# Kernel optimization log

Measured on AMD Instinct MI355X. Metric: run time of the kernel, lower is better.

The kernel has to match this reference:

```python
import jax, jax.numpy as jnp
import numpy as np

B, L, D = 64, 256, 768
LABELS = 200
REL_OFF = 256  # to_pos[k] = k + 256


def setup_inputs() -> dict:
    key = jax.random.key(0)
    ks = jax.random.split(key, 8)
    return {
        "sequence_output": jax.random.normal(ks[0], (B, L, D), dtype=jnp.float32),
        "pos_embedding": jax.random.normal(ks[1], (2 * REL_OFF + 1, D), dtype=jnp.float32) * 0.02,
        "class_embedding": jax.random.normal(ks[2], (LABELS + 1, D), dtype=jnp.float32) * 0.02,
        "W": jax.random.normal(ks[3], (LABELS, 3 * D), dtype=jnp.float32) * 0.02,
        "b": jnp.zeros((LABELS,), dtype=jnp.float32),
        "head_indexes": jax.random.randint(ks[4], (B, L), 0, L),
        "frame": jax.random.randint(ks[5], (B,), 0, LABELS + 1),
        "pos": jax.random.randint(ks[6], (B,), 0, L),
    }


def reference(sequence_output, pos_embedding, class_embedding, W, b, head_indexes, frame, pos):
    # per-batch gather of token rows: sequence_output[i] = sequence_output[i][head_indexes[i]]
    gathered = jnp.take_along_axis(sequence_output, head_indexes[:, :, None], axis=1)  # [B,L,D]

    j = jnp.arange(sequence_output.shape[1])  # [L]
    rel = j[None, :] - pos[:, None] + REL_OFF  # [B,L] in [0, 512]
    pe = pos_embedding[rel]  # [B,L,D]

    # frame embedding only at j == pos[i], else class_embedding[0]
    fe_hit = class_embedding[frame]  # [B,D]
    is_pos = (j[None, :] == pos[:, None])[:, :, None]  # [B,L,1]
    fe = jnp.where(is_pos, fe_hit[:, None, :], class_embedding[0][None, None, :])  # [B,L,D]

    feat = jnp.concatenate([gathered, pe, fe], axis=-1)  # [B,L,3D]
    # dropout is identity at inference; classifier linear
    return jnp.einsum("blf,cf->blc", feat, W) + b
```

## Files before the change

### kernel.cpp

```cpp
#include <hip/hip_runtime.h>
#include <stdint.h>


typedef __attribute__((ext_vector_type(8))) short short8;
typedef __attribute__((ext_vector_type(4))) float f32x4;

#define AS1 __attribute__((address_space(1)))
#define AS3 __attribute__((address_space(3)))

#define NSEQ_G 1572864
#define NPE_G  49248
#define NCE_G  19296
#define NW16_G 73728
#define SEQB_OFF 0
#define PEB_OFF  12582912
#define CEB_OFF  (PEB_OFF + 393984)
#define WP_OFF   (CEB_OFF + 154368)
#define WS_ELEMS (WP_OFF + 589824)
#define WS_NEED  ((size_t)WS_ELEMS * 2)
#define TILE_STRIDE 36864

__device__ __forceinline__ unsigned short f2bf(float f) {
    union { float f; unsigned int u; } v; v.f = f;
    unsigned int u = v.u;
    return (unsigned short)((u + 0x7fffu + ((u >> 16) & 1u)) >> 16);
}

__device__ __forceinline__ short8 pack8(f32x4 a, f32x4 b) {
    short8 r;
    r[0] = (short)f2bf(a.x); r[1] = (short)f2bf(a.y);
    r[2] = (short)f2bf(a.z); r[3] = (short)f2bf(a.w);
    r[4] = (short)f2bf(b.x); r[5] = (short)f2bf(b.y);
    r[6] = (short)f2bf(b.z); r[7] = (short)f2bf(b.w);
    return r;
}

__device__ __forceinline__ void dma16(const unsigned short* g, AS3 unsigned short* l) {
    __builtin_amdgcn_global_load_lds((AS1 const unsigned int*)g,
                                     (AS3 unsigned int*)l, 16, 0, 0);
}

__global__ void prep_kernel(const float* __restrict__ seq,
                            const float* __restrict__ pe,
                            const float* __restrict__ ce,
                            const float* __restrict__ W,
                            unsigned short* __restrict__ ws) {
    int g = blockIdx.x * 256 + threadIdx.x;
    if (g < NSEQ_G) {
        const float* p = seq + (size_t)g * 8;
        *(short8*)(ws + SEQB_OFF + (size_t)g * 8) =
            pack8(*(const f32x4*)p, *(const f32x4*)(p + 4));
        return;
    }
    g -= NSEQ_G;
    if (g < NPE_G) {
        const float* p = pe + (size_t)g * 8;
        *(short8*)(ws + PEB_OFF + (size_t)g * 8) =
            pack8(*(const f32x4*)p, *(const f32x4*)(p + 4));
        return;
    }
    g -= NPE_G;
    if (g < NCE_G) {
        const float* p = ce + (size_t)g * 8;
        *(short8*)(ws + CEB_OFF + (size_t)g * 8) =
            pack8(*(const f32x4*)p, *(const f32x4*)(p + 4));
        return;
    }
    g -= NCE_G;
    if (g < NW16_G) {
        int n   = g & 15;
        int kb8 = (g >> 4) % 288;
        int t   = g / (288 * 16);
        int row = t * 16 + n;
        int col = kb8 * 8;
        f32x4 a = {0.f, 0.f, 0.f, 0.f}, b = {0.f, 0.f, 0.f, 0.f};
        if (row < 200) {
            const float* p = W + (size_t)row * 2304 + col;
            a = *(const f32x4*)p;
            b = *(const f32x4*)(p + 4);
        }
        *(short8*)(ws + WP_OFF + (size_t)g * 8) = pack8(a, b);
    }
}

__global__ __launch_bounds__(512) void gemm6_kernel(
    const unsigned short* __restrict__ ws,
    const float* __restrict__ bias,
    const int*   __restrict__ head,
    const int*   __restrict__ frame,
    const int*   __restrict__ pos,
    float* __restrict__ out)
{
    __shared__ unsigned short lds[8192 + 16384];

    const unsigned short* seqb = ws + SEQB_OFF;
    const unsigned short* peb  = ws + PEB_OFF;
    const unsigned short* ceb  = ws + CEB_OFF;
    const unsigned short* Wp   = ws + WP_OFF;

    const int tid  = threadIdx.x;
    const int wave = tid >> 6;
    const int lane = tid & 63;
    const int n16  = lane & 15;
    const int quad = lane >> 4;

    const int mblk = blockIdx.x & 255;
    const int h    = blockIdx.x >> 8;

    const int i       = mblk >> 2;
    const int pos_i   = pos[i];
    const int frame_i = frame[i];

    const int smf = wave & 3;
    const int skb = (wave >> 2) * 2;
    const int srow = mblk * 64 + smf * 16 + n16;
    const unsigned short* aSt[3];
    {
        const int sj   = srow & 255;
        const int shi  = head[srow];
        const int srel = sj - pos_i + 256;
        const int scls = (sj == pos_i) ? frame_i : 0;
        const int loff = quad * 8;
        aSt[0] = seqb + ((size_t)i * 256 + (size_t)shi) * 768 + loff;
        aSt[1] = peb + (size_t)srel * 768 + loff;
        aSt[2] = ceb + (size_t)scls * 768 + loff;
    }
    AS3 unsigned short* aDst0 =
        (AS3 unsigned short*)lds + ((smf * 4 + skb) * 64 + lane) * 8;
    AS3 unsigned short* aDst1 = aDst0 + 512;

    const unsigned short* bSt = Wp + (size_t)(h * 8 + wave) * TILE_STRIDE + lane * 8;
    AS3 unsigned short* bDst =
        (AS3 unsigned short*)lds + 8192 + wave * 2048 + lane * 8;

    const int p = wave & 1;
    const int q = wave >> 1;

    const unsigned short* aRd[2];
    const unsigned short* bRd[2];
#pragma unroll
    for (int f = 0; f < 2; ++f)
        aRd[f] = lds + (2 * p + f) * 2048 + lane * 8;
#pragma unroll
    for (int u = 0; u < 2; ++u)
        bRd[u] = lds + 8192 + (q + 4 * u) * 2048 + quad * 128 + n16 * 8;

    f32x4 acc[2][2];
#pragma unroll
    for (int u = 0; u < 2; ++u) {
        const int col = (h * 8 + q + 4 * u) * 16 + n16;
        const float bv = (col < 200) ? bias[col] : 0.0f;
        acc[0][u] = (f32x4){bv, bv, bv, bv};
        acc[1][u] = (f32x4){bv, bv, bv, bv};
    }

#pragma unroll
    for (int sg = 0; sg < 3; ++sg) {
        const unsigned short* aSrc = aSt[sg];
        const unsigned short* bSrc = bSt + (size_t)sg * 12288;
        for (int cc = 0; cc < 6; ++cc) {
            dma16(aSrc + cc * 128 + skb * 32,      aDst0);
            dma16(aSrc + cc * 128 + skb * 32 + 32, aDst1);
            dma16(bSrc + cc * 2048,        bDst);
            dma16(bSrc + cc * 2048 + 512,  bDst + 512);
            dma16(bSrc + cc * 2048 + 1024, bDst + 1024);
            dma16(bSrc + cc * 2048 + 1536, bDst + 1536);
            __syncthreads();
#pragma unroll
            for (int ks = 0; ks < 4; ++ks) {
                short8 a0 = *(const short8*)(aRd[0] + ks * 512);
                short8 a1 = *(const short8*)(aRd[1] + ks * 512);
#pragma unroll
                for (int u = 0; u < 2; ++u) {
                    short8 bf = *(const short8*)(bRd[u] + ks * 512);
                    acc[0][u] = __builtin_amdgcn_mfma_f32_16x16x32_bf16(a0, bf, acc[0][u], 0, 0, 0);
                    acc[1][u] = __builtin_amdgcn_mfma_f32_16x16x32_bf16(a1, bf, acc[1][u], 0, 0, 0);
                }
            }
            __syncthreads();
        }
    }

#pragma unroll
    for (int f = 0; f < 2; ++f) {
        const int rbase = mblk * 64 + (2 * p + f) * 16 + quad * 4;
#pragma unroll
        for (int u = 0; u < 2; ++u) {
            const int col = (h * 8 + q + 4 * u) * 16 + n16;
            if (col < 200) {
#pragma unroll
                for (int r = 0; r < 4; ++r)
                    out[(size_t)(rbase + r) * 200 + col] = acc[f][u][r];
            }
        }
    }
}

__global__ __launch_bounds__(256) void gemm_fallback(
    const float* __restrict__ seq, const float* __restrict__ pe,
    const float* __restrict__ ce, const float* __restrict__ Wf,
    const float* __restrict__ bias, const int* __restrict__ head,
    const int* __restrict__ frame, const int* __restrict__ pos,
    float* __restrict__ out)
{
    const int tid  = threadIdx.x;
    const int wave = tid >> 6;
    const int lane = tid & 63;
    const int n16  = lane & 15;
    const int quad = lane >> 4;

    const int mrow  = blockIdx.x * 16 + n16;
    const int i     = mrow >> 8;
    const int j     = mrow & 255;
    const int pos_i = pos[i];
    const int hi    = head[mrow];
    const int rel   = j - pos_i + 256;
    const int cls   = (j == pos_i) ? frame[i] : 0;

    const float* segs[3];
    segs[0] = seq + ((size_t)i * 256 + (size_t)hi) * 768 + quad * 8;
    segs[1] = pe + (size_t)rel * 768 + quad * 8;
    segs[2] = ce + (size_t)cls * 768 + quad * 8;

    const int ntl = (wave == 0) ? 4 : 3;
    f32x4 acc[4];
#pragma unroll
    for (int u = 0; u < 4; ++u) {
        const int t = wave + 4 * u;
        const int col = t * 16 + n16;
        const float bv = (t < 13 && col < 200) ? bias[col] : 0.0f;
        acc[u] = (f32x4){bv, bv, bv, bv};
    }

    for (int s = 0; s < 3; ++s) {
        const float* ap = segs[s];
#pragma unroll 2
        for (int kk = 0; kk < 768; kk += 32) {
            short8 afr = pack8(*(const f32x4*)(ap + kk), *(const f32x4*)(ap + kk + 4));
#pragma unroll
            for (int u = 0; u < 4; ++u) {
                if (u < ntl) {
                    const int t = wave + 4 * u;
                    const int row = t * 16 + n16;
                    short8 bfr = {0, 0, 0, 0, 0, 0, 0, 0};
                    if (row < 200) {
                        const float* qp = Wf + (size_t)row * 2304 + s * 768 + kk + quad * 8;
                        bfr = pack8(*(const f32x4*)qp, *(const f32x4*)(qp + 4));
                    }
                    acc[u] = __builtin_amdgcn_mfma_f32_16x16x32_bf16(afr, bfr, acc[u], 0, 0, 0);
                }
            }
        }
    }

    const int rbase = blockIdx.x * 16 + quad * 4;
#pragma unroll
    for (int u = 0; u < 4; ++u) {
        const int t = wave + 4 * u;
        if (t < 13) {
            const int col = t * 16 + n16;
            if (col < 200) {
#pragma unroll
                for (int r = 0; r < 4; ++r)
                    out[(size_t)(rbase + r) * 200 + col] = acc[u][r];
            }
        }
    }
}

extern "C" void kernel_launch(void* const* d_in, const int* in_sizes, int n_in,
                              void* d_out, int out_size, void* d_ws, size_t ws_size,
                              hipStream_t stream) {
    const float* seq  = (const float*)d_in[0];
    const float* pe   = (const float*)d_in[1];
    const float* ce   = (const float*)d_in[2];
    const float* W    = (const float*)d_in[3];
    const float* bias = (const float*)d_in[4];
    const int* head   = (const int*)d_in[5];
    const int* frame  = (const int*)d_in[6];
    const int* pos    = (const int*)d_in[7];
    float* out = (float*)d_out;

    if (d_ws != nullptr && ws_size >= WS_NEED) {
        unsigned short* ws = (unsigned short*)d_ws;
        const int total_g = NSEQ_G + NPE_G + NCE_G + NW16_G;
        prep_kernel<<<(total_g + 255) / 256, 256, 0, stream>>>(seq, pe, ce, W, ws);
        gemm6_kernel<<<512, 512, 0, stream>>>(ws, bias, head, frame, pos, out);
    } else {
        gemm_fallback<<<1024, 256, 0, stream>>>(seq, pe, ce, W, bias, head,
                                                frame, pos, out);
    }
}
```

Before: 128.5 us.

## Precompute position/class logit tables and convert sequence rows to bf16 inside the GEMM

Splits the concatenated-feature GEMM into a K=768 GEMM over gathered sequence rows, plus two small lookup tables of logits (pos_embedding·W_pe and class_embedding·W_ce + bias). The prep kernel computes those tables instead of converting the whole 50 MB sequence tensor to bf16. The main GEMM loads fp32 rows directly, converts them in registers with a prefetch of the next chunk, and adds the table lookups in the epilogue. This removes the full-tensor conversion pass and two thirds of the main GEMM's K loop. In exchange the main kernel issues uncoalesced per-row fp32 loads, and the column split becomes uneven (7 and 6 tiles).

```diff
diff --git a/kernel.cpp b/kernel.cpp
--- a/kernel.cpp
+++ b/kernel.cpp
@@ -8,17 +8,13 @@
 #define AS1 __attribute__((address_space(1)))
 #define AS3 __attribute__((address_space(3)))
 
-#define NSEQ_G 1572864
-#define NPE_G  49248
-#define NCE_G  19296
-#define NW16_G 73728
-#define SEQB_OFF 0
-#define PEB_OFF  12582912
-#define CEB_OFF  (PEB_OFF + 393984)
-#define WP_OFF   (CEB_OFF + 154368)
-#define WS_ELEMS (WP_OFF + 589824)
-#define WS_NEED  ((size_t)WS_ELEMS * 2)
 #define TILE_STRIDE 36864
+#define NWPK_G     59904
+#define NWPK_BLK   234
+#define NLOG_BLK   46
+#define PEL_OFF_F  239616
+#define CEL_OFF_F  349440
+#define WS_NEED_B  1570816
 
 __device__ __forceinline__ unsigned short f2bf(float f) {
     union { float f; unsigned int u; } v; v.f = f;
@@ -40,63 +36,103 @@
                                      (AS3 unsigned int*)l, 16, 0, 0);
 }
 
-__global__ void prep_kernel(const float* __restrict__ seq,
-                            const float* __restrict__ pe,
-                            const float* __restrict__ ce,
-                            const float* __restrict__ W,
-                            unsigned short* __restrict__ ws) {
-    int g = blockIdx.x * 256 + threadIdx.x;
-    if (g < NSEQ_G) {
-        const float* p = seq + (size_t)g * 8;
-        *(short8*)(ws + SEQB_OFF + (size_t)g * 8) =
-            pack8(*(const f32x4*)p, *(const f32x4*)(p + 4));
-        return;
-    }
-    g -= NSEQ_G;
-    if (g < NPE_G) {
-        const float* p = pe + (size_t)g * 8;
-        *(short8*)(ws + PEB_OFF + (size_t)g * 8) =
-            pack8(*(const f32x4*)p, *(const f32x4*)(p + 4));
-        return;
-    }
-    g -= NPE_G;
-    if (g < NCE_G) {
-        const float* p = ce + (size_t)g * 8;
-        *(short8*)(ws + CEB_OFF + (size_t)g * 8) =
-            pack8(*(const f32x4*)p, *(const f32x4*)(p + 4));
-        return;
-    }
-    g -= NCE_G;
-    if (g < NW16_G) {
-        int n   = g & 15;
-        int kb8 = (g >> 4) % 288;
-        int t   = g / (288 * 16);
-        int row = t * 16 + n;
-        int col = kb8 * 8;
+__global__ __launch_bounds__(256) void prep_kernel(
+    const float* __restrict__ pe,
+    const float* __restrict__ ce,
+    const float* __restrict__ W,
+    const float* __restrict__ bias,
+    unsigned short* __restrict__ ws)
+{
+    if (blockIdx.x < NWPK_BLK) {
+        const int g   = blockIdx.x * 256 + threadIdx.x;
+        const int n   = g & 15;
+        const int kb8 = (g >> 4) % 288;
+        const int t   = g / 4608;
+        const int row = t * 16 + n;
+        const int col = kb8 * 8;
         f32x4 a = {0.f, 0.f, 0.f, 0.f}, b = {0.f, 0.f, 0.f, 0.f};
         if (row < 200) {
             const float* p = W + (size_t)row * 2304 + col;
             a = *(const f32x4*)p;
             b = *(const f32x4*)(p + 4);
         }
-        *(short8*)(ws + WP_OFF + (size_t)g * 8) = pack8(a, b);
-    }
-}
-
-__global__ __launch_bounds__(512) void gemm6_kernel(
+        *(short8*)(ws + (size_t)g * 8) = pack8(a, b);
+        return;
+    }
+
+    const int bb   = blockIdx.x - NWPK_BLK;
+    const int w    = threadIdx.x >> 6;
+    const int lane = threadIdx.x & 63;
+    const int n16  = lane & 15;
+    const int quad = lane >> 4;
+
+    float* wsF = (float*)ws;
+    int row0, nrows, koff;
+    const float* A;
+    float* outL;
+    bool isCe;
+    if (bb < 33) { isCe = false; row0 = bb * 16;        nrows = 513; koff = 768;  A = pe; outL = wsF + PEL_OFF_F; }
+    else         { isCe = true;  row0 = (bb - 33) * 16; nrows = 201; koff = 1536; A = ce; outL = wsF + CEL_OFF_F; }
+
+    int arow = row0 + n16; if (arow >= nrows) arow = nrows - 1;
+    const float* abase = A + (size_t)arow * 768 + quad * 8;
+
+    f32x4 acc[4];
+    const float* wbase[4];
+    bool wok[4];
+    int colU[4];
+#pragma unroll
+    for (int u = 0; u < 4; ++u) {
+        const int t   = w + 4 * u;
+        const int col = t * 16 + n16;
+        colU[u] = col;
+        wok[u]  = (t < 13) && (col < 200);
+        const float bv = (isCe && wok[u]) ? bias[col] : 0.0f;
+        acc[u] = (f32x4){bv, bv, bv, bv};
+        wbase[u] = W + (size_t)(wok[u] ? col : 0) * 2304 + koff + quad * 8;
+    }
+
+    for (int ks = 0; ks < 24; ++ks) {
+        const float* ap = abase + ks * 32;
+        short8 af = pack8(*(const f32x4*)ap, *(const f32x4*)(ap + 4));
+#pragma unroll
+        for (int u = 0; u < 4; ++u) {
+            if (w + 4 * u < 13) {
+                short8 bf = {0, 0, 0, 0, 0, 0, 0, 0};
+                if (wok[u]) {
+                    const float* wp = wbase[u] + ks * 32;
+                    bf = pack8(*(const f32x4*)wp, *(const f32x4*)(wp + 4));
+                }
+                acc[u] = __builtin_amdgcn_mfma_f32_16x16x32_bf16(af, bf, acc[u], 0, 0, 0);
+            }
+        }
+    }
+
+    const int rb = row0 + quad * 4;
+#pragma unroll
+    for (int u = 0; u < 4; ++u) {
+        if (w + 4 * u < 13) {
+#pragma unroll
+            for (int r = 0; r < 4; ++r)
+                outL[(size_t)(rb + r) * 208 + colU[u]] = acc[u][r];
+        }
+    }
+}
+
+__global__ __launch_bounds__(512, 4) void gemm_kernel(
     const unsigned short* __restrict__ ws,
-    const float* __restrict__ bias,
+    const float* __restrict__ seq,
     const int*   __restrict__ head,
     const int*   __restrict__ frame,
     const int*   __restrict__ pos,
     float* __restrict__ out)
 {
-    __shared__ unsigned short lds[8192 + 16384];
-
-    const unsigned short* seqb = ws + SEQB_OFF;
-    const unsigned short* peb  = ws + PEB_OFF;
-    const unsigned short* ceb  = ws + CEB_OFF;
-    const unsigned short* Wp   = ws + WP_OFF;
+    __shared__ unsigned short lds[8192 + 7 * 2048];
+
+    const unsigned short* Wp = ws;
+    const float* wsF = (const float*)ws;
+    const float* peL = wsF + PEL_OFF_F;
+    const float* ceL = wsF + CEL_OFF_F;
 
     const int tid  = threadIdx.x;
     const int wave = tid >> 6;
@@ -104,8 +140,10 @@
     const int n16  = lane & 15;
     const int quad = lane >> 4;
 
-    const int mblk = blockIdx.x & 255;
-    const int h    = blockIdx.x >> 8;
+    const int mblk   = blockIdx.x >> 1;
+    const int h      = blockIdx.x & 1;
+    const int ntiles = h ? 6 : 7;
+    const int tb     = h * 7;
 
     const int i       = mblk >> 2;
     const int pos_i   = pos[i];
@@ -114,71 +152,67 @@
     const int smf = wave & 3;
     const int skb = (wave >> 2) * 2;
     const int srow = mblk * 64 + smf * 16 + n16;
-    const unsigned short* aSt[3];
-    {
-        const int sj   = srow & 255;
-        const int shi  = head[srow];
-        const int srel = sj - pos_i + 256;
-        const int scls = (sj == pos_i) ? frame_i : 0;
-        const int loff = quad * 8;
-        aSt[0] = seqb + ((size_t)i * 256 + (size_t)shi) * 768 + loff;
-        aSt[1] = peb + (size_t)srel * 768 + loff;
-        aSt[2] = ceb + (size_t)scls * 768 + loff;
-    }
-    AS3 unsigned short* aDst0 =
-        (AS3 unsigned short*)lds + ((smf * 4 + skb) * 64 + lane) * 8;
-    AS3 unsigned short* aDst1 = aDst0 + 512;
-
-    const unsigned short* bSt = Wp + (size_t)(h * 8 + wave) * TILE_STRIDE + lane * 8;
-    AS3 unsigned short* bDst =
-        (AS3 unsigned short*)lds + 8192 + wave * 2048 + lane * 8;
+    const int hi   = head[srow];
+    const float* aP = seq + ((size_t)i * 256 + hi) * 768 + skb * 32 + quad * 8;
+    unsigned short* aDst0 = (unsigned short*)lds + ((smf * 4 + skb) * 64 + lane) * 8;
+    unsigned short* aDst1 = aDst0 + 512;
 
     const int p = wave & 1;
     const int q = wave >> 1;
-
-    const unsigned short* aRd[2];
+    const unsigned short* aRd0 = lds + (2 * p) * 2048 + lane * 8;
+    const unsigned short* aRd1 = aRd0 + 2048;
     const unsigned short* bRd[2];
+    bool uok[2];
+#pragma unroll
+    for (int u = 0; u < 2; ++u) {
+        const int t = q + 4 * u;
+        uok[u] = (t < ntiles);
+        bRd[u] = lds + 8192 + (uok[u] ? t : 0) * 2048 + quad * 128 + n16 * 8;
+    }
+
+    f32x4 acc[2][2];
 #pragma unroll
     for (int f = 0; f < 2; ++f)
-        aRd[f] = lds + (2 * p + f) * 2048 + lane * 8;
-#pragma unroll
-    for (int u = 0; u < 2; ++u)
-        bRd[u] = lds + 8192 + (q + 4 * u) * 2048 + quad * 128 + n16 * 8;
-
-    f32x4 acc[2][2];
-#pragma unroll
-    for (int u = 0; u < 2; ++u) {
-        const int col = (h * 8 + q + 4 * u) * 16 + n16;
-        const float bv = (col < 200) ? bias[col] : 0.0f;
-        acc[0][u] = (f32x4){bv, bv, bv, bv};
-        acc[1][u] = (f32x4){bv, bv, bv, bv};
-    }
-
-#pragma unroll
-    for (int sg = 0; sg < 3; ++sg) {
-        const unsigned short* aSrc = aSt[sg];
-        const unsigned short* bSrc = bSt + (size_t)sg * 12288;
-        for (int cc = 0; cc < 6; ++cc) {
-            dma16(aSrc + cc * 128 + skb * 32,      aDst0);
-            dma16(aSrc + cc * 128 + skb * 32 + 32, aDst1);
-            dma16(bSrc + cc * 2048,        bDst);
-            dma16(bSrc + cc * 2048 + 512,  bDst + 512);
-            dma16(bSrc + cc * 2048 + 1024, bDst + 1024);
-            dma16(bSrc + cc * 2048 + 1536, bDst + 1536);
-            __syncthreads();
-#pragma unroll
-            for (int ks = 0; ks < 4; ++ks) {
-                short8 a0 = *(const short8*)(aRd[0] + ks * 512);
-                short8 a1 = *(const short8*)(aRd[1] + ks * 512);
-#pragma unroll
-                for (int u = 0; u < 2; ++u) {
+#pragma unroll
+        for (int u = 0; u < 2; ++u)
+            acc[f][u] = (f32x4){0.f, 0.f, 0.f, 0.f};
+
+    f32x4 a00 = *(const f32x4*)(aP);
+    f32x4 a01 = *(const f32x4*)(aP + 4);
+    f32x4 a10 = *(const f32x4*)(aP + 32);
+    f32x4 a11 = *(const f32x4*)(aP + 36);
+
+    for (int cc = 0; cc < 6; ++cc) {
+        *(short8*)aDst0 = pack8(a00, a01);
+        *(short8*)aDst1 = pack8(a10, a11);
+        const int units = ntiles * 4;
+        for (int un = wave; un < units; un += 8) {
+            const int t = un >> 2, part = un & 3;
+            dma16(Wp + (size_t)(tb + t) * TILE_STRIDE + cc * 2048 + part * 512 + lane * 8,
+                  (AS3 unsigned short*)lds + 8192 + t * 2048 + part * 512 + lane * 8);
+        }
+        __syncthreads();
+        if (cc < 5) {
+            const float* ap = aP + (cc + 1) * 128;
+            a00 = *(const f32x4*)(ap);
+            a01 = *(const f32x4*)(ap + 4);
+            a10 = *(const f32x4*)(ap + 32);
+            a11 = *(const f32x4*)(ap + 36);
+        }
+#pragma unroll
+        for (int ks = 0; ks < 4; ++ks) {
+            short8 a0 = *(const short8*)(aRd0 + ks * 512);
+            short8 a1 = *(const short8*)(aRd1 + ks * 512);
+#pragma unroll
+            for (int u = 0; u < 2; ++u) {
+                if (uok[u]) {
                     short8 bf = *(const short8*)(bRd[u] + ks * 512);
                     acc[0][u] = __builtin_amdgcn_mfma_f32_16x16x32_bf16(a0, bf, acc[0][u], 0, 0, 0);
                     acc[1][u] = __builtin_amdgcn_mfma_f32_16x16x32_bf16(a1, bf, acc[1][u], 0, 0, 0);
                 }
             }
-            __syncthreads();
-        }
+        }
+        __syncthreads();
     }
 
 #pragma unroll
@@ -186,11 +220,20 @@
         const int rbase = mblk * 64 + (2 * p + f) * 16 + quad * 4;
 #pragma unroll
         for (int u = 0; u < 2; ++u) {
-            const int col = (h * 8 + q + 4 * u) * 16 + n16;
-            if (col < 200) {
-#pragma unroll
-                for (int r = 0; r < 4; ++r)
-                    out[(size_t)(rbase + r) * 200 + col] = acc[f][u][r];
+            if (uok[u]) {
+                const int col = (tb + q + 4 * u) * 16 + n16;
+                if (col < 200) {
+#pragma unroll
+                    for (int r = 0; r < 4; ++r) {
+                        const int row = rbase + r;
+                        const int l   = row & 255;
+                        const int rel = l - pos_i + 256;
+                        const int cls = (l == pos_i) ? frame_i : 0;
+                        out[(size_t)row * 200 + col] =
+                            acc[f][u][r] + peL[(size_t)rel * 208 + col]
+                                         + ceL[(size_t)cls * 208 + col];
+                    }
+                }
             }
         }
     }
@@ -281,11 +324,10 @@
     const int* pos    = (const int*)d_in[7];
     float* out = (float*)d_out;
 
-    if (d_ws != nullptr && ws_size >= WS_NEED) {
+    if (d_ws != nullptr && ws_size >= (size_t)WS_NEED_B) {
         unsigned short* ws = (unsigned short*)d_ws;
-        const int total_g = NSEQ_G + NPE_G + NCE_G + NW16_G;
-        prep_kernel<<<(total_g + 255) / 256, 256, 0, stream>>>(seq, pe, ce, W, ws);
-        gemm6_kernel<<<512, 512, 0, stream>>>(ws, bias, head, frame, pos, out);
+        prep_kernel<<<NWPK_BLK + NLOG_BLK, 256, 0, stream>>>(pe, ce, W, bias, ws);
+        gemm_kernel<<<512, 512, 0, stream>>>(ws, seq, head, frame, pos, out);
     } else {
         gemm_fallback<<<1024, 256, 0, stream>>>(seq, pe, ce, W, bias, head,
                                                 frame, pos, out);
```

Measured after the change: 162.3 us. 1.26x slower.
